# Performance work log

Hardware: AMD Instinct MI355X
Metric: run time of the kernel (lower is better)

The kernel has to match this reference:

```python
import math
import jax, jax.numpy as jnp
import numpy as np

GROUPS = 32
EPS = 1e-5


def group_norm(x, gamma, beta):
    # x: (b, c, h, w); normalize per-group over (c/g, h, w)
    b, c, h, w = x.shape
    xg = x.reshape(b, GROUPS, c // GROUPS, h, w)
    mu = xg.mean(axis=(2, 3, 4), keepdims=True)
    var = xg.var(axis=(2, 3, 4), keepdims=True)
    xn = ((xg - mu) * jax.lax.rsqrt(var + EPS)).reshape(b, c, h, w)
    return xn * gamma[None, :, None, None] + beta[None, :, None, None]


def conv1x1(x, w, bias):
    # x: (b, c, h, w), w: (o, c) -> (b, o, h, w)
    return jnp.einsum('bchw,oc->bohw', x, w) + bias[None, :, None, None]


def setup_inputs() -> dict:
    key = jax.random.key(0)
    ks = jax.random.split(key, 7)
    b, c, h, w = 8, 512, 32, 32
    s = 1.0 / math.sqrt(c)
    return {
        'x': jax.random.normal(ks[0], (b, c, h, w), dtype=jnp.float32),
        'gn_w': jnp.ones((c,), dtype=jnp.float32),
        'gn_b': jnp.zeros((c,), dtype=jnp.float32),
        'qkv_w': jax.random.normal(ks[1], (3 * c, c), dtype=jnp.float32) * s,
        'qkv_b': jnp.zeros((3 * c,), dtype=jnp.float32),
        'proj_w': jax.random.normal(ks[2], (c, c), dtype=jnp.float32) * s,
        'proj_b': jnp.zeros((c,), dtype=jnp.float32),
        'num_heads': 8,
    }


def reference(x, gn_w, gn_b, qkv_w, qkv_b, proj_w, proj_b, num_heads):
    b, c, h, w = x.shape
    hds = num_heads
    d = c // hds
    x_ = group_norm(x, gn_w, gn_b)
    qkv = conv1x1(x_, qkv_w, qkv_b)  # (b, 3c, h, w)
    q, k, v = jnp.split(qkv, 3, axis=1)
    # (b, hds, d, hw)
    q = q.reshape(b, hds, d, h * w)
    k = k.reshape(b, hds, d, h * w)
    v = v.reshape(b, hds, d, h * w)
    # scores: (b, hds, hw, hw) = q^T k / sqrt(d)
    scores = jnp.einsum('bhdq,bhdk->bhqk', q, k) / math.sqrt(d)
    attn = jax.nn.softmax(scores, axis=-1)
    # out = (attn @ v^T)^T -> (b, hds, d, hw)
    out = jnp.einsum('bhqk,bhdk->bhdq', attn, v)
    out = out.reshape(b, c, h, w)
    return x + conv1x1(out, proj_w, proj_b)
```

## Files before the change

kernel.cpp:

```cpp
#include <hip/hip_runtime.h>
#include <hip/hip_bf16.h>


typedef __attribute__((ext_vector_type(8))) short short8v;
typedef __attribute__((ext_vector_type(4))) short short4v;
typedef __attribute__((ext_vector_type(4))) float f32x4;
typedef __attribute__((ext_vector_type(2))) unsigned uint2v;
typedef __attribute__((ext_vector_type(4))) unsigned uint4v;

constexpr int Bn = 8, Cn = 512, HWn = 1024;

#if __has_builtin(__builtin_amdgcn_exp2f)
#define EXP2F(x) __builtin_amdgcn_exp2f(x)
#else
#define EXP2F(x) __exp2f(x)
#endif

static __device__ __forceinline__ unsigned short bf16u(float f) {
  __hip_bfloat16 h = __float2bfloat16(f);
  return __builtin_bit_cast(unsigned short, h);
}
static __device__ __forceinline__ short bf16_of(float f) {
  return (short)bf16u(f);
}
static __device__ __forceinline__ unsigned bf16pk(float a, float b) {
  return (unsigned)bf16u(a) | ((unsigned)bf16u(b) << 16);
}

static __device__ __forceinline__ void gload16(const void* g, void* l) {
  __builtin_amdgcn_global_load_lds(
      (const __attribute__((address_space(1))) unsigned*)g,
      (__attribute__((address_space(3))) unsigned*)l, 16, 0, 0);
}

__global__ __launch_bounds__(256) void gn_fused_k(const float* __restrict__ x,
                                                  const float* __restrict__ gw,
                                                  const float* __restrict__ gb,
                                                  const float* __restrict__ wq,
                                                  const float* __restrict__ wp,
                                                  short* __restrict__ oq,
                                                  short* __restrict__ op,
                                                  short* __restrict__ xn3) {
  const int t = threadIdx.x;
  if (blockIdx.x >= 256) {
    int i = (blockIdx.x - 256) * 256 + t;
    const float* src = wq;
    short* dst = oq;
    int idx = i;
    if (i >= 196608) { src = wp; dst = op; idx = i - 196608; }
    f32x4 v = ((const f32x4*)src)[idx];
    short4v o;
    o.x = bf16_of(v.x); o.y = bf16_of(v.y); o.z = bf16_of(v.z); o.w = bf16_of(v.w);
    *(short4v*)&dst[idx * 4] = o;
    return;
  }
  const int bg = blockIdx.x;
  const int g = bg & 31;
  const f32x4* src = (const f32x4*)(x + (size_t)bg * 16384);
  f32x4 v[16];
  float s = 0.f, ss = 0.f;
#pragma unroll
  for (int k = 0; k < 16; k++) {
    v[k] = src[t + 256 * k];
    s += v[k].x + v[k].y + v[k].z + v[k].w;
    ss += v[k].x * v[k].x + v[k].y * v[k].y + v[k].z * v[k].z + v[k].w * v[k].w;
  }
#pragma unroll
  for (int off = 32; off; off >>= 1) {
    s += __shfl_xor(s, off);
    ss += __shfl_xor(ss, off);
  }
  __shared__ float rs[4], rss[4];
  const int lane = t & 63, w = t >> 6;
  if (lane == 0) { rs[w] = s; rss[w] = ss; }
  __syncthreads();
  const float S = rs[0] + rs[1] + rs[2] + rs[3];
  const float SS = rss[0] + rss[1] + rss[2] + rss[3];
  constexpr float invn = 1.0f / 16384.f;
  const float mu = S * invn;
  const float var = SS * invn - mu * mu;
  const float rstd = rsqrtf(var + 1e-5f);
  float ga[16], be[16];
#pragma unroll
  for (int k = 0; k < 16; k++) {
    ga[k] = gw[g * 16 + k] * rstd;
    be[k] = gb[g * 16 + k] - mu * ga[k];
  }
  short* dst = xn3 + (size_t)bg * 16384;
#pragma unroll
  for (int d = 0; d < 4; d++) {
    unsigned pk[8];
#pragma unroll
    for (int k = 0; k < 16; k += 2)
      pk[k >> 1] = bf16pk(fmaf(v[k][d], ga[k], be[k]),
                          fmaf(v[k + 1][d], ga[k + 1], be[k + 1]));
    uint4v lo = {pk[0], pk[1], pk[2], pk[3]};
    uint4v hi = {pk[4], pk[5], pk[6], pk[7]};
    *(uint4v*)&dst[(4 * t + d) * 16] = lo;
    *(uint4v*)&dst[(4 * t + d) * 16 + 8] = hi;
  }
}

__device__ __forceinline__ short8v frag64(const short* buf, int row, int gk) {
  return *(const short8v*)&buf[row * 64 + ((gk ^ (row & 7)) << 3)];
}

__global__ __launch_bounds__(256, 2) void gemm_qkv_k(
    const short* __restrict__ A, const short* __restrict__ xn3,
    const float* __restrict__ bias, short* __restrict__ oQ,
    short* __restrict__ oK, short* __restrict__ oV) {
  const int bid = blockIdx.x;
  const int swz = (bid & 7) * 96 + (bid >> 3);
  const int bn = swz & 7;
  const int rest = swz >> 3;
  const int bm = rest % 12, b = rest / 12;
  const bool VBLK = (bm >= 8);

  const short* Bb = xn3 + (size_t)b * 524288;
  __shared__ __align__(16) short As[2][8192];
  __shared__ __align__(16) short Bs[2][8192];
  const int t = threadIdx.x, l = t & 63, w = t >> 6;
  const int wr = w >> 1, wc = w & 1;
  const int m0 = bm * 128, n0 = bn * 128;
  const f32x4 vzero = {0.f, 0.f, 0.f, 0.f};
  f32x4 acc[4][4];
#pragma unroll
  for (int i = 0; i < 4; i++)
#pragma unroll
    for (int j = 0; j < 4; j++) acc[i][j] = vzero;

  const int sr0 = t >> 3;
  const int sg = t & 7;

#define STAGE_QKV(buf, k0)                                                    \
  do {                                                                        \
    _Pragma("unroll") for (int it = 0; it < 4; it++) {                        \
      int r = it * 32 + sr0;                                                  \
      int gs = sg ^ (r & 7);                                                  \
      gload16(&A[(size_t)(m0 + r) * 512 + (k0) + gs * 8],                     \
              &As[buf][it * 2048 + w * 512]);                                 \
      int gp = ((k0) >> 4) + (gs >> 1);                                       \
      gload16(&Bb[(size_t)((gp << 10) + n0 + r) * 16 + ((gs & 1) << 3)],      \
              &Bs[buf][it * 2048 + w * 512]);                                 \
    }                                                                         \
  } while (0)

  STAGE_QKV(0, 0);
  __syncthreads();

  for (int ks = 0; ks < 8; ks++) {
    const int cb = ks & 1;
    if (ks < 7) STAGE_QKV(cb ^ 1, (ks + 1) * 64);
#pragma unroll
    for (int kk = 0; kk < 2; kk++) {
      short8v af[4], bf[4];
#pragma unroll
      for (int i = 0; i < 4; i++)
        af[i] = frag64(&As[cb][0], wr * 64 + i * 16 + (l & 15), kk * 4 + (l >> 4));
#pragma unroll
      for (int j = 0; j < 4; j++)
        bf[j] = frag64(&Bs[cb][0], wc * 64 + j * 16 + (l & 15), kk * 4 + (l >> 4));
      if (VBLK) {
#pragma unroll
        for (int i = 0; i < 4; i++)
#pragma unroll
          for (int j = 0; j < 4; j++)
            acc[i][j] = __builtin_amdgcn_mfma_f32_16x16x32_bf16(bf[j], af[i], acc[i][j], 0, 0, 0);
      } else {
#pragma unroll
        for (int i = 0; i < 4; i++)
#pragma unroll
          for (int j = 0; j < 4; j++)
            acc[i][j] = __builtin_amdgcn_mfma_f32_16x16x32_bf16(af[i], bf[j], acc[i][j], 0, 0, 0);
      }
    }
    __syncthreads();
  }

  if (!VBLK) {
    short* oBase = (m0 < 512) ? oQ : oK;
    const int mc = (m0 < 512 ? m0 : m0 - 512) + wr * 64;
#pragma unroll
    for (int i = 0; i < 4; i++) {
      int mi = mc + i * 16 + (l >> 4) * 4;
      f32x4 bv = *(const f32x4*)&bias[m0 + wr * 64 + i * 16 + (l >> 4) * 4];
#pragma unroll
      for (int j = 0; j < 4; j++) {
        int n = n0 + wc * 64 + j * 16 + (l & 15);
        uint2v pk = {bf16pk(acc[i][j][0] + bv[0], acc[i][j][1] + bv[1]),
                     bf16pk(acc[i][j][2] + bv[2], acc[i][j][3] + bv[3])};
        *(uint2v*)&oBase[((size_t)b * HWn + n) * 512 + mi] = pk;
      }
    }
  } else {
#pragma unroll
    for (int i = 0; i < 4; i++) {
      int m = m0 + wr * 64 + i * 16 + (l & 15);
      float bv = bias[m];
      short* vrow = oV + ((size_t)b * 512 + (m - 1024)) * HWn;
#pragma unroll
      for (int j = 0; j < 4; j++) {
        int n = n0 + wc * 64 + j * 16 + (l >> 4) * 4;
        uint2v pk = {bf16pk(acc[i][j][0] + bv, acc[i][j][1] + bv),
                     bf16pk(acc[i][j][2] + bv, acc[i][j][3] + bv)};
        *(uint2v*)&vrow[n] = pk;
      }
    }
  }
}

__global__ __launch_bounds__(512, 2) void gemm_proj_k(
    const short* __restrict__ A, const short* __restrict__ Bt,
    const float* __restrict__ bias, const float* __restrict__ resid,
    float* __restrict__ outF) {
  const int bid = blockIdx.x;
  const int swz = (bid & 7) * 32 + (bid >> 3);
  const int bn = swz & 7;
  const int rest = swz >> 3;
  const int bm = rest & 3, b = rest >> 2;

  const short* Bb = Bt + (size_t)b * HWn * Cn;
  __shared__ __align__(16) short As[2][8192];
  __shared__ __align__(16) short Bs[2][8192];
  const int t = threadIdx.x, l = t & 63, w = t >> 6;
  const int wr = w >> 1, wc = w & 1;
  const int m0 = bm * 128, n0 = bn * 128;
  const f32x4 vzero = {0.f, 0.f, 0.f, 0.f};
  f32x4 acc[2][4];
#pragma unroll
  for (int i = 0; i < 2; i++)
#pragma unroll
    for (int j = 0; j < 4; j++) acc[i][j] = vzero;

  const int sr0 = t >> 3;
  const int sg = t & 7;

#define STAGE_PROJ(buf, k0)                                                   \
  do {                                                                        \
    _Pragma("unroll") for (int it = 0; it < 2; it++) {                        \
      int r = it * 64 + sr0;                                                  \
      int gs = sg ^ (r & 7);                                                  \
      gload16(&A[(size_t)(m0 + r) * 512 + (k0) + gs * 8],                     \
              &As[buf][it * 4096 + w * 512]);                                 \
      gload16(&Bb[(size_t)(n0 + r) * 512 + (k0) + gs * 8],                    \
              &Bs[buf][it * 4096 + w * 512]);                                 \
    }                                                                         \
  } while (0)

  STAGE_PROJ(0, 0);
  __syncthreads();

  for (int ks = 0; ks < 8; ks++) {
    const int cb = ks & 1;
    if (ks < 7) STAGE_PROJ(cb ^ 1, (ks + 1) * 64);
#pragma unroll
    for (int kk = 0; kk < 2; kk++) {
      short8v af[2], bf[4];
#pragma unroll
      for (int i = 0; i < 2; i++)
        af[i] = frag64(&As[cb][0], wr * 32 + i * 16 + (l & 15), kk * 4 + (l >> 4));
#pragma unroll
      for (int j = 0; j < 4; j++)
        bf[j] = frag64(&Bs[cb][0], wc * 64 + j * 16 + (l & 15), kk * 4 + (l >> 4));
#pragma unroll
      for (int i = 0; i < 2; i++)
#pragma unroll
        for (int j = 0; j < 4; j++)
          acc[i][j] = __builtin_amdgcn_mfma_f32_16x16x32_bf16(af[i], bf[j], acc[i][j], 0, 0, 0);
    }
    __syncthreads();
  }

  float* outb = outF + (size_t)b * Cn * HWn;
  const float* rb = resid + (size_t)b * Cn * HWn;
#pragma unroll
  for (int i = 0; i < 2; i++) {
    f32x4 bv = *(const f32x4*)&bias[m0 + wr * 32 + i * 16 + (l >> 4) * 4];
#pragma unroll
    for (int r = 0; r < 4; r++) {
      int m = m0 + wr * 32 + i * 16 + (l >> 4) * 4 + r;
#pragma unroll
      for (int j = 0; j < 4; j++) {
        int n = n0 + wc * 64 + j * 16 + (l & 15);
        size_t idx = (size_t)m * HWn + n;
        outb[idx] = acc[i][j][r] + bv[r] + rb[idx];
      }
    }
  }
}

__global__ __launch_bounds__(256, 3) void attn_k(const short* __restrict__ qT,
                                                 const short* __restrict__ kT,
                                                 const short* __restrict__ vB,
                                                 short* __restrict__ aoT) {
  const int bid = blockIdx.x;
  const int swz = (bid & 7) * 64 + (bid >> 3);
  const int qt = swz & 7, head = (swz >> 3) & 7, b = swz >> 6;
  __shared__ __align__(16) short SM[17408];
  short* Ks = SM;
  short* Vs = SM + 4096;
  short* Ps = SM + 8192;
  const int t = threadIdx.x, l = t & 63, w = t >> 6;
  short* PsA = Ps + (2 * w) * 1152;
  short* PsB = Ps + (2 * w + 1) * 1152;
  const int g = l >> 4;
  const f32x4 vzero = {0.f, 0.f, 0.f, 0.f};

  const short* ksrc = kT + (size_t)b * HWn * 512 + head * 64;
  const short* vsrc = vB + ((size_t)b * 512 + head * 64) * HWn;

  const short* qbase = qT +
      ((size_t)b * HWn + qt * 128 + 32 * w + (l & 15)) * 512 + head * 64 + g * 8;
  const short8v qA0 = *(const short8v*)&qbase[0];
  const short8v qA1 = *(const short8v*)&qbase[32];
  const short8v qB0 = *(const short8v*)&qbase[16 * 512];
  const short8v qB1 = *(const short8v*)&qbase[16 * 512 + 32];

  const int sr = t >> 3, sg = t & 7;

  f32x4 oaA[4], oaB[4];
#pragma unroll
  for (int f = 0; f < 4; f++) { oaA[f] = vzero; oaB[f] = vzero; }
  float lA = 0.f, lB = 0.f;
  constexpr float SC = 0.1803368801111f;
  constexpr float MOFF = -11.5415602855f;

#pragma unroll 1
  for (int kt = 0; kt < 16; kt++) {
    __syncthreads();
#pragma unroll
    for (int it = 0; it < 2; it++) {
      int kv = it * 32 + sr;
      gload16(&ksrc[(size_t)(kt * 64 + kv) * 512 + (sg ^ (kv & 7)) * 8],
              &Ks[it * 2048 + w * 512]);
      int d = it * 32 + sr;
      gload16(&vsrc[(size_t)d * HWn + kt * 64 + (sg ^ (d & 7)) * 8],
              &Vs[it * 2048 + w * 512]);
    }
    __syncthreads();

    f32x4 saA[4], saB[4];
    __builtin_amdgcn_s_setprio(1);
#pragma unroll
    for (int f = 0; f < 4; f++) {
      short8v ka0 = frag64(Ks, 16 * f + (l & 15), g);
      short8v ka1 = frag64(Ks, 16 * f + (l & 15), g + 4);
      saA[f] = __builtin_amdgcn_mfma_f32_16x16x32_bf16(ka0, qA0, vzero, 0, 0, 0);
      saB[f] = __builtin_amdgcn_mfma_f32_16x16x32_bf16(ka0, qB0, vzero, 0, 0, 0);
      saA[f] = __builtin_amdgcn_mfma_f32_16x16x32_bf16(ka1, qA1, saA[f], 0, 0, 0);
      saB[f] = __builtin_amdgcn_mfma_f32_16x16x32_bf16(ka1, qB1, saB[f], 0, 0, 0);
    }
    __builtin_amdgcn_s_setprio(0);

    f32x4 psAv = vzero, psBv = vzero;
#pragma unroll
    for (int f = 0; f < 4; f++)
#pragma unroll
      for (int r = 0; r < 4; r++) {
        float eA = EXP2F(fmaf(saA[f][r], SC, MOFF));
        float eB = EXP2F(fmaf(saB[f][r], SC, MOFF));
        saA[f][r] = eA;
        saB[f][r] = eB;
        psAv[r] += eA;
        psBv[r] += eB;
      }
    float psA = (psAv[0] + psAv[1]) + (psAv[2] + psAv[3]);
    float psB = (psBv[0] + psBv[1]) + (psBv[2] + psBv[3]);
    psA += __shfl_xor(psA, 16);
    psA += __shfl_xor(psA, 32);
    psB += __shfl_xor(psB, 16);
    psB += __shfl_xor(psB, 32);
    lA += psA;
    lB += psB;

#pragma unroll
    for (int f = 0; f < 4; f++) {
      int o = (l & 15) * 72 + 16 * f + 4 * g;
      uint2v pkA = {bf16pk(saA[f][0], saA[f][1]), bf16pk(saA[f][2], saA[f][3])};
      uint2v pkB = {bf16pk(saB[f][0], saB[f][1]), bf16pk(saB[f][2], saB[f][3])};
      *(uint2v*)&PsA[o] = pkA;
      *(uint2v*)&PsB[o] = pkB;
    }
    short8v paA[2], paB[2];
#pragma unroll
    for (int c = 0; c < 2; c++) {
      paA[c] = *(const short8v*)&PsA[(l & 15) * 72 + c * 32 + g * 8];
      paB[c] = *(const short8v*)&PsB[(l & 15) * 72 + c * 32 + g * 8];
    }
    __builtin_amdgcn_s_setprio(1);
#pragma unroll
    for (int fd = 0; fd < 4; fd++) {
      int row = 16 * fd + (l & 15);
#pragma unroll
      for (int c = 0; c < 2; c++) {
        short8v vb = frag64(Vs, row, c * 4 + g);
        oaA[fd] = __builtin_amdgcn_mfma_f32_16x16x32_bf16(paA[c], vb, oaA[fd], 0, 0, 0);
        oaB[fd] = __builtin_amdgcn_mfma_f32_16x16x32_bf16(paB[c], vb, oaB[fd], 0, 0, 0);
      }
    }
    __builtin_amdgcn_s_setprio(0);
  }

  const float invA = 1.0f / lA, invB = 1.0f / lB;
  float ivA[4], ivB[4];
#pragma unroll
  for (int r = 0; r < 4; r++) {
    ivA[r] = __shfl(invA, 4 * g + r);
    ivB[r] = __shfl(invB, 4 * g + r);
  }
  __syncthreads();
#pragma unroll
  for (int r = 0; r < 4; r++)
#pragma unroll
    for (int f = 0; f < 4; f++) {
      PsA[(4 * g + r) * 72 + 16 * f + (l & 15)] = bf16_of(oaA[f][r] * ivA[r]);
      PsB[(4 * g + r) * 72 + 16 * f + (l & 15)] = bf16_of(oaB[f][r] * ivB[r]);
    }
  __syncthreads();
  short* dst = aoT + ((size_t)b * HWn + qt * 128) * 512 + head * 64;
#pragma unroll
  for (int it = 0; it < 4; it++) {
    int r = (t >> 3) + 32 * it;
    int c8 = (t & 7) * 8;
    *(short8v*)&dst[(size_t)r * 512 + c8] =
        *(const short8v*)&Ps[(r >> 4) * 1152 + (r & 15) * 72 + c8];
  }
}

extern "C" void kernel_launch(void* const* d_in, const int* in_sizes, int n_in,
                              void* d_out, int out_size, void* d_ws, size_t ws_size,
                              hipStream_t stream) {
  const float* x = (const float*)d_in[0];
  const float* gn_w = (const float*)d_in[1];
  const float* gn_b = (const float*)d_in[2];
  const float* qkv_w = (const float*)d_in[3];
  const float* qkv_b = (const float*)d_in[4];
  const float* proj_w = (const float*)d_in[5];
  const float* proj_b = (const float*)d_in[6];
  float* out = (float*)d_out;

  char* ws = (char*)d_ws;
  short* wqb = (short*)(ws + 4096);
  short* wpb = (short*)(ws + 4096 + 1572864);
  char* p = ws + 4096 + 1572864 + 524288;
  const size_t SB = (size_t)Bn * HWn * 512 * 2;
  short* xn3 = (short*)p;
  short* qT = (short*)(p + SB);
  short* kT = (short*)(p + 2 * SB);
  short* vB = (short*)(p + 3 * SB);
  short* aoT = (short*)(p + 4 * SB);

  gn_fused_k<<<1280, 256, 0, stream>>>(x, gn_w, gn_b, qkv_w, proj_w, wqb, wpb, xn3);
  gemm_qkv_k<<<768, 256, 0, stream>>>(wqb, xn3, qkv_b, qT, kT, vB);
  attn_k<<<512, 256, 0, stream>>>(qT, kT, vB, aoT);
  gemm_proj_k<<<256, 512, 0, stream>>>(wpb, aoT, proj_b, x, out);
}
```

Measured before the change: 80.25 us.

## Single-buffer QKV GEMM shared tiles to raise occupancy to three blocks

Drops the double-buffered LDS staging in the QKV projection GEMM and uses one A/B tile pair, loading each K-slab and syncing before the MFMA loop. The launch bound is raised from 2 to 3 blocks per CU, since halving shared memory per block allows more resident blocks. This gives up overlap of global loads with compute inside a block in exchange for more blocks hiding latency. The loop also appears to lack a barrier after compute before the next overwrite, which could be a race unless one survives in unseen code.

```diff
diff --git a/kernel.cpp b/kernel.cpp
--- a/kernel.cpp
+++ b/kernel.cpp
@@ -105,7 +105,7 @@
   return *(const short8v*)&buf[row * 64 + ((gk ^ (row & 7)) << 3)];
 }
 
-__global__ __launch_bounds__(256, 2) void gemm_qkv_k(
+__global__ __launch_bounds__(256, 3) void gemm_qkv_k(
     const short* __restrict__ A, const short* __restrict__ xn3,
     const float* __restrict__ bias, short* __restrict__ oQ,
     short* __restrict__ oK, short* __restrict__ oV) {
@@ -117,8 +117,8 @@
   const bool VBLK = (bm >= 8);
 
   const short* Bb = xn3 + (size_t)b * 524288;
-  __shared__ __align__(16) short As[2][8192];
-  __shared__ __align__(16) short Bs[2][8192];
+  __shared__ __align__(16) short As[8192];
+  __shared__ __align__(16) short Bs[8192];
   const int t = threadIdx.x, l = t & 63, w = t >> 6;
   const int wr = w >> 1, wc = w & 1;
   const int m0 = bm * 128, n0 = bn * 128;
@@ -132,34 +132,26 @@
   const int sr0 = t >> 3;
   const int sg = t & 7;
 
-#define STAGE_QKV(buf, k0)                                                    \
-  do {                                                                        \
-    _Pragma("unroll") for (int it = 0; it < 4; it++) {                        \
-      int r = it * 32 + sr0;                                                  \
-      int gs = sg ^ (r & 7);                                                  \
-      gload16(&A[(size_t)(m0 + r) * 512 + (k0) + gs * 8],                     \
-              &As[buf][it * 2048 + w * 512]);                                 \
-      int gp = ((k0) >> 4) + (gs >> 1);                                       \
-      gload16(&Bb[(size_t)((gp << 10) + n0 + r) * 16 + ((gs & 1) << 3)],      \
-              &Bs[buf][it * 2048 + w * 512]);                                 \
-    }                                                                         \
-  } while (0)
-
-  STAGE_QKV(0, 0);
-  __syncthreads();
-
-  for (int ks = 0; ks < 8; ks++) {
-    const int cb = ks & 1;
-    if (ks < 7) STAGE_QKV(cb ^ 1, (ks + 1) * 64);
+  for (int k0 = 0; k0 < 512; k0 += 64) {
+#pragma unroll
+    for (int it = 0; it < 4; it++) {
+      int r = it * 32 + sr0;
+      int gs = sg ^ (r & 7);
+      gload16(&A[(size_t)(m0 + r) * 512 + k0 + gs * 8], &As[it * 2048 + w * 512]);
+      int gp = (k0 >> 4) + (gs >> 1);
+      gload16(&Bb[(size_t)((gp << 10) + n0 + r) * 16 + ((gs & 1) << 3)],
+              &Bs[it * 2048 + w * 512]);
+    }
+    __syncthreads();
 #pragma unroll
     for (int kk = 0; kk < 2; kk++) {
       short8v af[4], bf[4];
 #pragma unroll
       for (int i = 0; i < 4; i++)
-        af[i] = frag64(&As[cb][0], wr * 64 + i * 16 + (l & 15), kk * 4 + (l >> 4));
+        af[i] = frag64(As, wr * 64 + i * 16 + (l & 15), kk * 4 + (l >> 4));
 #pragma unroll
       for (int j = 0; j < 4; j++)
-        bf[j] = frag64(&Bs[cb][0], wc * 64 + j * 16 + (l & 15), kk * 4 + (l >> 4));
+        bf[j] = frag64(Bs, wc * 64 + j * 16 + (l & 15), kk * 4 + (l >> 4));
       if (VBLK) {
 #pragma unroll
         for (int i = 0; i < 4; i++)
```

Result: slower. 103.1 us (+28.5%).
